# Performance work log

Measured on AMD Instinct MI355X. Metric: run time of the kernel, lower is better.

Reference implementation:

```python
import jax, jax.numpy as jnp
import numpy as np

B, L, D, NH = 4, 1500, 512, 8
HD = D // NH
EPS = 1e-8            # F.normalize eps
PEPS = 1.1920929e-07  # torch clamp_probs eps for float32
TEMP = 1.0


def setup_inputs():
    key = jax.random.key(0)
    ks = jax.random.split(key, 12)
    s = 1.0 / np.sqrt(D)
    eye = jnp.eye(D, dtype=jnp.float32)
    return {
        "hidden": jax.random.normal(ks[0], (B, L, D), jnp.float32),
        "lengths": jnp.ones((B,), jnp.float32),
        "u_noise": jax.random.uniform(ks[1], (B, L), jnp.float32),
        "W1": jax.random.normal(ks[2], (D, D), jnp.float32) * s,
        "b1": jnp.zeros((D,), jnp.float32),
        "W2": jax.random.normal(ks[3], (D, D), jnp.float32) * s,
        "b2": jnp.zeros((D,), jnp.float32),
        "Wq": eye + jax.random.normal(ks[4], (D, D), jnp.float32) * 0.01,
        "Wk": eye + jax.random.normal(ks[5], (D, D), jnp.float32) * 0.01,
        "sim_bias": jnp.float32(0.098),
        "learned_query": jax.random.normal(ks[6], (D,), jnp.float32),
        "Wpk": eye + jax.random.normal(ks[7], (D, D), jnp.float32) * 0.01,
        "Wpv": eye + jax.random.normal(ks[8], (D, D), jnp.float32) * 0.01,
        "Wpo": eye + jax.random.normal(ks[9], (D, D), jnp.float32) * 0.01,
        "ln_g": jnp.ones((D,), jnp.float32),
        "ln_b": jnp.zeros((D,), jnp.float32),
    }


def reference(hidden, lengths, u_noise, W1, b1, W2, b2, Wq, Wk, sim_bias,
              learned_query, Wpk, Wpv, Wpo, ln_g, ln_b):
    Bb, Ll, Dd = hidden.shape

    def nrm(x):
        n = jnp.sqrt(jnp.sum(x * x, -1, keepdims=True))
        return x / jnp.maximum(n, EPS)

    def mlp(x):
        return jax.nn.gelu(x @ W1.T + b1, approximate=False) @ W2.T + b2

    # boundary logits from adjacent-frame cosine similarity (dropout = eval identity)
    q_in = nrm(hidden[:, :-1]); q = nrm(mlp(q_in) + q_in) @ Wq.T
    k_in = nrm(hidden[:, 1:]);  k = nrm(mlp(k_in) + k_in) @ Wk.T
    cos = jnp.sum(q * k, -1)                                   # (B, L-1)
    probs = jnp.clip((1.0 - (cos + sim_bias)) * 0.5, 0.0, 1.0)
    probs = jnp.pad(probs, ((0, 0), (0, 1)))                   # (B, L)

    # RelaxedBernoulli rsample with explicit logistic noise
    p = jnp.clip(probs, PEPS, 1.0 - PEPS)
    u = jnp.clip(u_noise, PEPS, 1.0 - PEPS)
    soft = jax.nn.sigmoid((jnp.log(p) - jnp.log1p(-p) + jnp.log(u) - jnp.log1p(-u)) / TEMP)
    hard = (soft > 0.5).astype(hidden.dtype)

    idx = jnp.arange(Ll)
    valid_len = jnp.minimum((lengths * (Ll + 1)).astype(jnp.int32) - 1, Ll)
    trunc = (valid_len < Ll)[:, None]
    zmask = trunc & (idx[None] >= valid_len[:, None])
    omask = trunc & (idx[None] == valid_len[:, None])
    soft = jnp.where(omask, 1.0, jnp.where(zmask, 0.0, soft))
    hard = jnp.where(omask, 1.0, jnp.where(zmask, 0.0, hard))
    hard_b = hard - jax.lax.stop_gradient(soft) + soft         # straight-through
    # emergency boundary for all-zero rows
    no_b = (jnp.sum(hard, 1) == 0)[:, None]
    hard_b = jnp.where(no_b & (idx[None] == jnp.minimum(valid_len, Ll - 1)[:, None]), 1.0, hard_b)

    # segment membership (common()): token l in segment s iff exclusive cumsum == s
    seg = jnp.cumsum(hard_b, 1) - hard_b                       # (B, L)
    lmask = idx[None] < (lengths * Ll).astype(jnp.int32)[:, None]
    seg_mask = (seg[:, :, None] == idx[None, None, :].astype(hidden.dtype)) & lmask[:, :, None]  # (B,L,S)

    # layernorm + K/V projections
    mu = jnp.mean(hidden, -1, keepdims=True)
    hv = hidden - mu
    hn = hv / jnp.sqrt(jnp.mean(hv * hv, -1, keepdims=True) + 1e-5) * ln_g + ln_b
    keys = (hn @ Wpk.T).reshape(Bb, Ll, NH, HD)
    vals = (hn @ Wpv.T).reshape(Bb, Ll, NH, HD)

    # query is shared across segments -> scores only differ via the segment mask
    qh = learned_query.reshape(NH, HD)
    base = jnp.einsum('hd,blhd->bhl', qh, keys) * (HD ** -0.5)  # (B,H,L)
    mask_t = jnp.transpose(seg_mask, (0, 2, 1))[:, None]        # (B,1,S,L)
    sc = jnp.where(mask_t, base[:, :, None, :], -jnp.inf)       # (B,H,S,L)
    aw = jnp.nan_to_num(jax.nn.softmax(sc, axis=-1))            # empty segments -> 0 rows
    pooled = jnp.einsum('bhsl,blhd->bshd', aw, vals).reshape(Bb, Ll, Dd)
    return pooled @ Wpo.T                                       # (B, S=L, D)
```

## Files before the change

kernel.cpp:

```cpp
#include <hip/hip_runtime.h>
#include <math.h>

#define Bz 4
#define Lz 1500
#define Dz 512
#define NHz 8
#define Nz (Bz*Lz)
#define NRT 375
#define PEPSf 1.1920929e-07f

typedef __bf16 bf16x8 __attribute__((ext_vector_type(8)));
typedef unsigned short u16x8 __attribute__((ext_vector_type(8)));
typedef float f32x4 __attribute__((ext_vector_type(4)));
typedef unsigned short us;

__device__ __forceinline__ us f2bf(float f) {
  unsigned u = __float_as_uint(f);
  return (us)((u + 0x7fffu + ((u >> 16) & 1u)) >> 16);
}
__device__ __forceinline__ float bf2f(us b) {
  return __uint_as_float(((unsigned)b) << 16);
}
__device__ __forceinline__ void st_tiled(us* __restrict__ P, int row, int col, us v) {
  P[(((row >> 4) * 64 + (col >> 3)) << 7) + ((row & 15) << 3) + (col & 7)] = v;
}

__device__ __forceinline__ bool decode_blk(int bx, int ncg, int& R, int& cg) {
  int xcd = bx & 7, v = bx >> 3;
  cg = v % ncg;
  R = (v / ncg) * 8 + xcd;
  return R < 94;
}

__global__ __launch_bounds__(256) void k_wconv(
    const float* __restrict__ s0, const float* __restrict__ s1, const float* __restrict__ s2,
    const float* __restrict__ s3, const float* __restrict__ s4, const float* __restrict__ s5,
    us* __restrict__ h0, us* __restrict__ h1, us* __restrict__ h2,
    us* __restrict__ h3, us* __restrict__ h4, us* __restrict__ h5,
    us* __restrict__ l0, us* __restrict__ l1, us* __restrict__ l2, us* __restrict__ l3) {
  const int rt = blockIdx.x, mat = blockIdx.y, t = threadIdx.x;
  const float* S; us* H; us* L = nullptr;
  switch (mat) {
    case 0: S = s0; H = h0; L = l0; break;
    case 1: S = s1; H = h1; L = l1; break;
    case 2: S = s2; H = h2; L = l2; break;
    case 3: S = s3; H = h3; L = l3; break;
    case 4: S = s4; H = h4; break;
    default: S = s5; H = h5; break;
  }
  for (int e = t; e < 8192; e += 256) {
    int mm = e >> 9, c = e & 511;
    float x = S[(size_t)(rt * 16 + mm) * 512 + c];
    us hb = f2bf(x);
    int off = ((rt * 64 + (c >> 3)) << 7) + (mm << 3) + (c & 7);
    H[off] = hb;
    if (L) L[off] = f2bf(x - bf2f(hb));
  }
}

__global__ __launch_bounds__(256) void k_rowprep(const float* __restrict__ h,
    const float* __restrict__ g, const float* __restrict__ bb,
    float* __restrict__ U, float* __restrict__ HN,
    us* __restrict__ Uh, us* __restrict__ Ul, us* __restrict__ HNh) {
  const int row = blockIdx.x;
  const int t = threadIdx.x;
  const float* x = h + (size_t)row * Dz;
  float x0 = x[t], x1 = x[t + 256];
  float s = x0 + x1, q = x0 * x0 + x1 * x1;
  #pragma unroll
  for (int o = 32; o > 0; o >>= 1) { s += __shfl_xor(s, o, 64); q += __shfl_xor(q, o, 64); }
  __shared__ float ls[4], lq[4];
  if ((t & 63) == 0) { ls[t >> 6] = s; lq[t >> 6] = q; }
  __syncthreads();
  s = ls[0] + ls[1] + ls[2] + ls[3];
  q = lq[0] + lq[1] + lq[2] + lq[3];
  float un = 1.f / fmaxf(sqrtf(q), 1e-8f);
  float u0 = x0 * un, u1 = x1 * un;
  float* up = U + (size_t)row * Dz;
  up[t] = u0; up[t + 256] = u1;
  us hb0 = f2bf(u0), hb1 = f2bf(u1);
  st_tiled(Uh, row, t, hb0);       st_tiled(Ul, row, t, f2bf(u0 - bf2f(hb0)));
  st_tiled(Uh, row, t + 256, hb1); st_tiled(Ul, row, t + 256, f2bf(u1 - bf2f(hb1)));
  float mu = s * (1.f / 512.f);
  float var = fmaxf(q * (1.f / 512.f) - mu * mu, 0.f);
  float r = rsqrtf(var + 1e-5f);
  float hn0 = (x0 - mu) * r * g[t] + bb[t];
  float hn1 = (x1 - mu) * r * g[t + 256] + bb[t + 256];
  float* hp = HN + (size_t)row * Dz;
  hp[t] = hn0; hp[t + 256] = hn1;
  st_tiled(HNh, row, t, f2bf(hn0));
  st_tiled(HNh, row, t + 256, f2bf(hn1));
}

__global__ __launch_bounds__(256) void k_rownorm(const float* __restrict__ M,
    us* __restrict__ Vh, us* __restrict__ Vl) {
  const int row = blockIdx.x;
  const int t = threadIdx.x;
  const float* x = M + (size_t)row * Dz;
  float x0 = x[t], x1 = x[t + 256];
  float q = x0 * x0 + x1 * x1;
  #pragma unroll
  for (int o = 32; o > 0; o >>= 1) q += __shfl_xor(q, o, 64);
  __shared__ float lq[4];
  if ((t & 63) == 0) lq[t >> 6] = q;
  __syncthreads();
  q = lq[0] + lq[1] + lq[2] + lq[3];
  float un = 1.f / fmaxf(sqrtf(q), 1e-8f);
  float v0 = x0 * un, v1 = x1 * un;
  us hb0 = f2bf(v0), hb1 = f2bf(v1);
  st_tiled(Vh, row, t, hb0);       st_tiled(Vl, row, t, f2bf(v0 - bf2f(hb0)));
  st_tiled(Vh, row, t + 256, hb1); st_tiled(Vl, row, t + 256, f2bf(v1 - bf2f(hb1)));
}

template<int SPLIT>
__device__ __forceinline__ void gemm_body(
    const us* __restrict__ Ah, const us* __restrict__ Al,
    const us* __restrict__ Bh, const us* __restrict__ Bl,
    const float* __restrict__ bias, const float* __restrict__ addsrc, int doGelu,
    float* __restrict__ outF, us* __restrict__ outH, us* __restrict__ outL,
    int R, int cg, int colbase) {
  const int t = threadIdx.x, w = t >> 6, l = t & 63;
  const int m = l & 15, q = l >> 4;
  const int rt0 = R * 4;
  const int ct0 = cg * 8 + w * 2;
  const int laneoff = q * 128 + m * 8;

  const u16x8* pa[4]; const u16x8* pal[4];
  const u16x8* pb[2]; const u16x8* pbl[2];
  #pragma unroll
  for (int i = 0; i < 4; ++i) {
    int rt = min(rt0 + i, NRT - 1);
    pa[i] = (const u16x8*)(Ah + (size_t)rt * 8192 + laneoff);
    if (SPLIT == 3) pal[i] = (const u16x8*)(Al + (size_t)rt * 8192 + laneoff);
  }
  #pragma unroll
  for (int j = 0; j < 2; ++j) {
    pb[j] = (const u16x8*)(Bh + (size_t)(ct0 + j) * 8192 + laneoff);
    if (SPLIT == 3) pbl[j] = (const u16x8*)(Bl + (size_t)(ct0 + j) * 8192 + laneoff);
  }

  u16x8 bAh[2][4], bAl[2][4], bBh[2][2], bBl[2][2];
  #pragma unroll
  for (int i = 0; i < 4; ++i) {
    bAh[0][i] = pa[i][0];
    if (SPLIT == 3) bAl[0][i] = pal[i][0];
  }
  #pragma unroll
  for (int j = 0; j < 2; ++j) {
    bBh[0][j] = pb[j][0];
    if (SPLIT == 3) bBl[0][j] = pbl[j][0];
  }

  f32x4 acc[4][2];
  #pragma unroll
  for (int i = 0; i < 4; ++i)
    #pragma unroll
    for (int j = 0; j < 2; ++j) acc[i][j] = (f32x4){0.f, 0.f, 0.f, 0.f};

  #pragma unroll 2
  for (int s = 0; s < 16; ++s) {
    const int cur = s & 1, nxt = cur ^ 1;
    const int sn = (s + 1) & 15;
    #pragma unroll
    for (int i = 0; i < 4; ++i) {
      bAh[nxt][i] = pa[i][sn * 64];
      if (SPLIT == 3) bAl[nxt][i] = pal[i][sn * 64];
    }
    #pragma unroll
    for (int j = 0; j < 2; ++j) {
      bBh[nxt][j] = pb[j][sn * 64];
      if (SPLIT == 3) bBl[nxt][j] = pbl[j][sn * 64];
    }
    #pragma unroll
    for (int i = 0; i < 4; ++i)
      #pragma unroll
      for (int j = 0; j < 2; ++j) {
        bf16x8 a = __builtin_bit_cast(bf16x8, bAh[cur][i]);
        bf16x8 b = __builtin_bit_cast(bf16x8, bBh[cur][j]);
        acc[i][j] = __builtin_amdgcn_mfma_f32_16x16x32_bf16(a, b, acc[i][j], 0, 0, 0);
        if (SPLIT == 3) {
          bf16x8 al_ = __builtin_bit_cast(bf16x8, bAl[cur][i]);
          bf16x8 bl_ = __builtin_bit_cast(bf16x8, bBl[cur][j]);
          acc[i][j] = __builtin_amdgcn_mfma_f32_16x16x32_bf16(a, bl_, acc[i][j], 0, 0, 0);
          acc[i][j] = __builtin_amdgcn_mfma_f32_16x16x32_bf16(al_, b, acc[i][j], 0, 0, 0);
        }
      }
  }

  const int row0 = rt0 * 16;
  #pragma unroll
  for (int i = 0; i < 4; ++i) {
    #pragma unroll
    for (int r = 0; r < 4; ++r) {
      const int grow = row0 + i * 16 + q * 4 + r;
      if (grow >= Nz) continue;
      #pragma unroll
      for (int j = 0; j < 2; ++j) {
        const int gcol = colbase + (w * 2 + j) * 16 + m;
        float v = acc[i][j][r];
        if (bias)   v += bias[gcol];
        if (addsrc) v += addsrc[(size_t)grow * Dz + gcol];
        if (doGelu) v = 0.5f * v * (1.f + erff(v * 0.70710678118654752f));
        if (outF) outF[(size_t)grow * Dz + gcol] = v;
        if (outH) {
          us hb = f2bf(v);
          st_tiled(outH, grow, gcol, hb);
          if (outL) st_tiled(outL, grow, gcol, f2bf(v - bf2f(hb)));
        }
      }
    }
  }
}

__global__ __launch_bounds__(256, 2) void g_t1_vals(
    const us* Uh, const us* Ul, const us* W1h, const us* W1l, const float* b1, us* T1h, us* T1l,
    const us* HNh, const us* Wpvh, float* VALS) {
  int R, cg;
  if (!decode_blk(blockIdx.x, 4, R, cg)) return;
  if (blockIdx.z == 0)
    gemm_body<3>(Uh, Ul, W1h, W1l, b1, nullptr, 1, nullptr, T1h, T1l, R, cg, cg * 128);
  else
    gemm_body<1>(HNh, nullptr, Wpvh, nullptr, nullptr, nullptr, 0, VALS, nullptr, nullptr, R, cg, cg * 128);
}

__global__ __launch_bounds__(256, 2) void g_w2(
    const us* T1h, const us* T1l, const us* W2h, const us* W2l, const float* b2,
    const float* U, float* M) {
  int R, cg;
  if (!decode_blk(blockIdx.x, 4, R, cg)) return;
  gemm_body<3>(T1h, T1l, W2h, W2l, b2, U, 0, M, nullptr, nullptr, R, cg, cg * 128);
}

__global__ __launch_bounds__(256, 2) void g_qk(
    const us* Vh, const us* Vl, const us* Wqh, const us* Wql, const us* Wkh, const us* Wkl,
    float* QF, float* KF) {
  int R, cg;
  if (!decode_blk(blockIdx.x, 8, R, cg)) return;
  if (cg < 4)
    gemm_body<3>(Vh, Vl, Wqh, Wql, nullptr, nullptr, 0, QF, nullptr, nullptr, R, cg & 3, (cg & 3) * 128);
  else
    gemm_body<3>(Vh, Vl, Wkh, Wkl, nullptr, nullptr, 0, KF, nullptr, nullptr, R, cg & 3, (cg & 3) * 128);
}

__global__ __launch_bounds__(256, 2) void g_out(
    const us* Ph, const us* Wpoh, float* out) {
  int R, cg;
  if (!decode_blk(blockIdx.x, 4, R, cg)) return;
  gemm_body<1>(Ph, nullptr, Wpoh, nullptr, nullptr, nullptr, 0, out, nullptr, nullptr, R, cg, cg * 128);
}

__global__ void k_probs(const float* __restrict__ QF, const float* __restrict__ KF,
                        const float* __restrict__ simb, float* __restrict__ probs) {
  const int l = blockIdx.x, b = blockIdx.y, t = threadIdx.x;
  if (l == Lz - 1) { if (t == 0) probs[(size_t)b * Lz + l] = 0.f; return; }
  const float* qp = QF + ((size_t)b * Lz + l) * Dz;
  const float* kp = KF + ((size_t)b * Lz + l + 1) * Dz;
  float acc = 0.f;
  for (int i = t; i < Dz; i += 64) acc += qp[i] * kp[i];
  #pragma unroll
  for (int o = 32; o > 0; o >>= 1) acc += __shfl_xor(acc, o, 64);
  if (t == 0) {
    float p = (1.f - (acc + simb[0])) * 0.5f;
    probs[(size_t)b * Lz + l] = fminf(fmaxf(p, 0.f), 1.f);
  }
}

__global__ __launch_bounds__(256) void k_boundary(const float* __restrict__ probs,
    const float* __restrict__ un, const float* __restrict__ lengths,
    int* __restrict__ seg_start, int* __restrict__ seg_meta) {
  const int b = blockIdx.x, t = threadIdx.x;
  __shared__ float hard[Lz];
  __shared__ float ps[256];
  __shared__ float ws4[4];
  const float len = lengths[b];
  const int valid_len = min((int)(len * (Lz + 1)) - 1, Lz);
  const int Lm = (int)(len * Lz);
  const bool trunc = valid_len < Lz;
  for (int l = t; l < Lz; l += 256) {
    float p = probs[(size_t)b * Lz + l];
    p = fminf(fmaxf(p, PEPSf), 1.f - PEPSf);
    float u = un[(size_t)b * Lz + l];
    u = fminf(fmaxf(u, PEPSf), 1.f - PEPSf);
    float z = logf(p) - log1pf(-p) + logf(u) - log1pf(-u);
    float soft = 1.f / (1.f + expf(-z));
    float hd = soft > 0.5f ? 1.f : 0.f;
    if (trunc && l >= valid_len) hd = (l == valid_len) ? 1.f : 0.f;
    hard[l] = hd;
  }
  __syncthreads();
  float sm = 0.f;
  for (int l = t; l < Lz; l += 256) sm += hard[l];
  #pragma unroll
  for (int o = 32; o > 0; o >>= 1) sm += __shfl_xor(sm, o, 64);
  if ((t & 63) == 0) ws4[t >> 6] = sm;
  __syncthreads();
  float total = ws4[0] + ws4[1] + ws4[2] + ws4[3];
  if (total == 0.f && t == 0) hard[min(valid_len, Lz - 1)] = 1.f;
  __syncthreads();
  const int l0 = t * 6;
  float loc = 0.f;
  for (int i = 0; i < 6; ++i) { int l = l0 + i; if (l < Lz) loc += hard[l]; }
  ps[t] = loc;
  __syncthreads();
  for (int off = 1; off < 256; off <<= 1) {
    float v = (t >= off) ? ps[t - off] : 0.f;
    __syncthreads();
    ps[t] += v;
    __syncthreads();
  }
  float run = ps[t] - loc;
  for (int i = 0; i < 6; ++i) {
    int l = l0 + i; if (l >= Lz) break;
    int seg = (int)(run + 0.5f);
    if (l == 0) seg_start[b * (Lz + 1) + 0] = 0;
    else if (hard[l - 1] > 0.5f) seg_start[b * (Lz + 1) + seg] = l;
    if (l == Lz - 1) {
      int nseg = seg + 1;
      seg_meta[b * 2 + 0] = nseg;
      seg_meta[b * 2 + 1] = Lm;
      seg_start[b * (Lz + 1) + nseg] = Lz;
    }
    run += hard[l];
  }
}

__global__ void k_wqeff(const float* __restrict__ lq, const float* __restrict__ Wpk,
                        float* __restrict__ wqe) {
  const int h = blockIdx.x, d = threadIdx.x;
  float acc = 0.f;
  for (int e = 0; e < 64; ++e) acc += lq[h * 64 + e] * Wpk[(size_t)(h * 64 + e) * Dz + d];
  wqe[h * Dz + d] = acc;
}

__global__ __launch_bounds__(256) void k_base(const float* __restrict__ HN,
    const float* __restrict__ wqe, float* __restrict__ base) {
  const int row = blockIdx.x, t = threadIdx.x;
  __shared__ float xs[Dz];
  xs[t] = HN[(size_t)row * Dz + t];
  xs[t + 256] = HN[(size_t)row * Dz + t + 256];
  __syncthreads();
  const int h = t >> 5, lane = t & 31;
  float acc = 0.f;
  for (int d = lane; d < Dz; d += 32) acc += xs[d] * wqe[h * Dz + d];
  #pragma unroll
  for (int o = 16; o > 0; o >>= 1) acc += __shfl_xor(acc, o, 32);
  if (lane == 0) base[(size_t)row * NHz + h] = acc * 0.125f;
}

__global__ __launch_bounds__(256) void k_pool(const float* __restrict__ base,
    const float* __restrict__ VALS, const int* __restrict__ seg_start,
    const int* __restrict__ seg_meta, us* __restrict__ Ph) {
  const int s = blockIdx.x, b = blockIdx.y, t = threadIdx.x;
  const int orow = b * Lz + s;
  const int nseg = seg_meta[b * 2], Lm = seg_meta[b * 2 + 1];
  int start = 0, end = 0;
  bool empty = true;
  if (s < nseg) {
    start = seg_start[b * (Lz + 1) + s];
    end = min(seg_start[b * (Lz + 1) + s + 1], Lm);
    empty = start >= end;
  }
  if (empty) { st_tiled(Ph, orow, t, 0); st_tiled(Ph, orow, t + 256, 0); return; }
  const int h = t >> 5, lane = t & 31;
  const float* bp = base + (size_t)b * Lz * NHz + h;
  float m = -1e30f;
  for (int l = start + lane; l < end; l += 32) m = fmaxf(m, bp[(size_t)l * NHz]);
  #pragma unroll
  for (int o = 16; o > 0; o >>= 1) m = fmaxf(m, __shfl_xor(m, o, 32));
  float den = 0.f;
  for (int l = start + lane; l < end; l += 32) den += expf(bp[(size_t)l * NHz] - m);
  #pragma unroll
  for (int o = 16; o > 0; o >>= 1) den += __shfl_xor(den, o, 32);
  float a0 = 0.f, a1 = 0.f;
  const float* vp = VALS + (size_t)b * Lz * Dz + h * 64 + lane;
  for (int l = start; l < end; ++l) {
    float wgt = expf(bp[(size_t)l * NHz] - m);
    a0 += wgt * vp[(size_t)l * Dz];
    a1 += wgt * vp[(size_t)l * Dz + 32];
  }
  float inv = 1.f / den;
  st_tiled(Ph, orow, h * 64 + lane, f2bf(a0 * inv));
  st_tiled(Ph, orow, h * 64 + lane + 32, f2bf(a1 * inv));
}

extern "C" void kernel_launch(void* const* d_in, const int* in_sizes, int n_in,
                              void* d_out, int out_size, void* d_ws, size_t ws_size,
                              hipStream_t stream) {
  const float* hidden  = (const float*)d_in[0];
  const float* lengths = (const float*)d_in[1];
  const float* unoise  = (const float*)d_in[2];
  const float* W1  = (const float*)d_in[3];
  const float* b1  = (const float*)d_in[4];
  const float* W2  = (const float*)d_in[5];
  const float* b2  = (const float*)d_in[6];
  const float* Wq  = (const float*)d_in[7];
  const float* Wk  = (const float*)d_in[8];
  const float* simb   = (const float*)d_in[9];
  const float* lquery = (const float*)d_in[10];
  const float* Wpk = (const float*)d_in[11];
  const float* Wpv = (const float*)d_in[12];
  const float* Wpo = (const float*)d_in[13];
  const float* lng = (const float*)d_in[14];
  const float* lnb = (const float*)d_in[15];
  float* out = (float*)d_out;

  char* p = (char*)d_ws;
  const size_t SF = (size_t)Nz * Dz * 4;
  const size_t TP = (size_t)376 * 8192 * 2;
  const size_t WP = (size_t)32 * 8192 * 2;
  float* U    = (float*)p; p += SF;
  float* HN   = (float*)p; p += SF;
  float* M    = (float*)p; p += SF;
  float* QF   = (float*)p; p += SF;
  float* KF   = (float*)p; p += SF;
  float* VALS = (float*)p; p += SF;
  us* Uh  = (us*)p; p += TP;
  us* Ul  = (us*)p; p += TP;
  us* T1h = (us*)p; p += TP;
  us* T1l = (us*)p; p += TP;
  us* Vh  = (us*)p; p += TP;
  us* Vl  = (us*)p; p += TP;
  us* HNh = (us*)p; p += TP;
  us* Ph  = (us*)p; p += TP;
  us* W1h = (us*)p; p += WP;
  us* W1l = (us*)p; p += WP;
  us* W2h = (us*)p; p += WP;
  us* W2l = (us*)p; p += WP;
  us* Wqh = (us*)p; p += WP;
  us* Wql = (us*)p; p += WP;
  us* Wkh = (us*)p; p += WP;
  us* Wkl = (us*)p; p += WP;
  us* Wpvh = (us*)p; p += WP;
  us* Wpoh = (us*)p; p += WP;
  float* probs  = (float*)p; p += 24064;
  float* base   = (float*)p; p += 192000;
  int* segst    = (int*)p;   p += 24064;
  int* segmeta  = (int*)p;   p += 256;
  float* wqe    = (float*)p;

  const int G4 = 8 * 12 * 4;
  const int G8 = 8 * 12 * 8;

  k_wconv<<<dim3(32, 6), 256, 0, stream>>>(W1, W2, Wq, Wk, Wpv, Wpo,
      W1h, W2h, Wqh, Wkh, Wpvh, Wpoh, W1l, W2l, Wql, Wkl);
  k_wqeff<<<NHz, 512, 0, stream>>>(lquery, Wpk, wqe);
  k_rowprep<<<Nz, 256, 0, stream>>>(hidden, lng, lnb, U, HN, Uh, Ul, HNh);
  g_t1_vals<<<dim3(G4, 1, 2), 256, 0, stream>>>(Uh, Ul, W1h, W1l, b1, T1h, T1l,
                                                HNh, Wpvh, VALS);
  g_w2<<<G4, 256, 0, stream>>>(T1h, T1l, W2h, W2l, b2, U, M);
  k_rownorm<<<Nz, 256, 0, stream>>>(M, Vh, Vl);
  g_qk<<<G8, 256, 0, stream>>>(Vh, Vl, Wqh, Wql, Wkh, Wkl, QF, KF);
  k_probs<<<dim3(Lz, Bz), 64, 0, stream>>>(QF, KF, simb, probs);
  k_boundary<<<Bz, 256, 0, stream>>>(probs, unoise, lengths, segst, segmeta);
  k_base<<<Nz, 256, 0, stream>>>(HN, wqe, base);
  k_pool<<<dim3(Lz, Bz), 256, 0, stream>>>(base, VALS, segst, segmeta, Ph);
  g_out<<<G4, 256, 0, stream>>>(Ph, Wpoh, out);
}
```

Measured before the change: 262.0 us.

## Fold Wq and Wk into one Gram matrix and fuse base into rowprep

Rewrites cos = (Wq v_l)·(Wk v_{l+1}) as v_l·(Wq^T Wk) M_{l+1}·rn. A small 512x512 GEMM precomputes G = Wq^T Wk, so the two large Q/K projection GEMMs become one GEMM plus a scaled dot with the unnormalized M. The k_base head-score reduction moves into k_rowprep, and the wqe computation moves into the weight conversion kernel, which removes two launches and a reread of HN. Launch bounds rise to 3 blocks per CU, and the extra bf16-split rounding of G may shift the probabilities near the hard threshold.

```diff
diff --git a/kernel.cpp b/kernel.cpp
--- a/kernel.cpp
+++ b/kernel.cpp
@@ -6,7 +6,6 @@
 #define Dz 512
 #define NHz 8
 #define Nz (Bz*Lz)
-#define NRT 375
 #define PEPSf 1.1920929e-07f
 
 typedef __bf16 bf16x8 __attribute__((ext_vector_type(8)));
@@ -34,23 +33,37 @@
 
 __global__ __launch_bounds__(256) void k_wconv(
     const float* __restrict__ s0, const float* __restrict__ s1, const float* __restrict__ s2,
-    const float* __restrict__ s3, const float* __restrict__ s4, const float* __restrict__ s5,
-    us* __restrict__ h0, us* __restrict__ h1, us* __restrict__ h2,
-    us* __restrict__ h3, us* __restrict__ h4, us* __restrict__ h5,
-    us* __restrict__ l0, us* __restrict__ l1, us* __restrict__ l2, us* __restrict__ l3) {
+    const float* __restrict__ s3,
+    const float* __restrict__ Wq, const float* __restrict__ Wk,
+    const float* __restrict__ Wpk, const float* __restrict__ lq,
+    us* __restrict__ h0, us* __restrict__ h1, us* __restrict__ h2, us* __restrict__ h3,
+    us* __restrict__ l0, us* __restrict__ l1,
+    us* __restrict__ WkTh, us* __restrict__ WkTl, us* __restrict__ WqTh, us* __restrict__ WqTl,
+    float* __restrict__ wqe) {
   const int rt = blockIdx.x, mat = blockIdx.y, t = threadIdx.x;
-  const float* S; us* H; us* L = nullptr;
+  if (mat == 8) {
+    if (rt < 8) {
+      for (int d = t; d < Dz; d += 256) {
+        float acc = 0.f;
+        for (int e = 0; e < 64; ++e) acc += lq[rt * 64 + e] * Wpk[(size_t)(rt * 64 + e) * Dz + d];
+        wqe[rt * Dz + d] = acc;
+      }
+    }
+    return;
+  }
+  const float* S; us* H; us* L = nullptr; bool tr = false;
   switch (mat) {
     case 0: S = s0; H = h0; L = l0; break;
     case 1: S = s1; H = h1; L = l1; break;
-    case 2: S = s2; H = h2; L = l2; break;
-    case 3: S = s3; H = h3; L = l3; break;
-    case 4: S = s4; H = h4; break;
-    default: S = s5; H = h5; break;
+    case 2: S = s2; H = h2; break;
+    case 3: S = s3; H = h3; break;
+    case 4: S = Wk; H = WkTh; L = WkTl; tr = true; break;
+    default: S = Wq; H = WqTh; L = WqTl; tr = true; break;
   }
   for (int e = t; e < 8192; e += 256) {
     int mm = e >> 9, c = e & 511;
-    float x = S[(size_t)(rt * 16 + mm) * 512 + c];
+    float x = tr ? S[(size_t)c * 512 + (rt * 16 + mm)]
+                 : S[(size_t)(rt * 16 + mm) * 512 + c];
     us hb = f2bf(x);
     int off = ((rt * 64 + (c >> 3)) << 7) + (mm << 3) + (c & 7);
     H[off] = hb;
@@ -60,8 +73,10 @@
 
 __global__ __launch_bounds__(256) void k_rowprep(const float* __restrict__ h,
     const float* __restrict__ g, const float* __restrict__ bb,
+    const float* __restrict__ wqe,
     float* __restrict__ U, float* __restrict__ HN,
-    us* __restrict__ Uh, us* __restrict__ Ul, us* __restrict__ HNh) {
+    us* __restrict__ Uh, us* __restrict__ Ul, us* __restrict__ HNh,
+    float* __restrict__ base) {
   const int row = blockIdx.x;
   const int t = threadIdx.x;
   const float* x = h + (size_t)row * Dz;
@@ -70,6 +85,7 @@
   #pragma unroll
   for (int o = 32; o > 0; o >>= 1) { s += __shfl_xor(s, o, 64); q += __shfl_xor(q, o, 64); }
   __shared__ float ls[4], lq[4];
+  __shared__ float xs[Dz];
   if ((t & 63) == 0) { ls[t >> 6] = s; lq[t >> 6] = q; }
   __syncthreads();
   s = ls[0] + ls[1] + ls[2] + ls[3];
@@ -90,10 +106,18 @@
   hp[t] = hn0; hp[t + 256] = hn1;
   st_tiled(HNh, row, t, f2bf(hn0));
   st_tiled(HNh, row, t + 256, f2bf(hn1));
+  xs[t] = hn0; xs[t + 256] = hn1;
+  __syncthreads();
+  const int hh = t >> 5, lane = t & 31;
+  float accb = 0.f;
+  for (int d = lane; d < Dz; d += 32) accb += xs[d] * wqe[hh * Dz + d];
+  #pragma unroll
+  for (int o = 16; o > 0; o >>= 1) accb += __shfl_xor(accb, o, 32);
+  if (lane == 0) base[(size_t)row * NHz + hh] = accb * 0.125f;
 }
 
 __global__ __launch_bounds__(256) void k_rownorm(const float* __restrict__ M,
-    us* __restrict__ Vh, us* __restrict__ Vl) {
+    us* __restrict__ Vh, us* __restrict__ Vl, float* __restrict__ rn) {
   const int row = blockIdx.x;
   const int t = threadIdx.x;
   const float* x = M + (size_t)row * Dz;
@@ -106,6 +130,7 @@
   __syncthreads();
   q = lq[0] + lq[1] + lq[2] + lq[3];
   float un = 1.f / fmaxf(sqrtf(q), 1e-8f);
+  if (t == 0) rn[row] = un;
   float v0 = x0 * un, v1 = x1 * un;
   us hb0 = f2bf(v0), hb1 = f2bf(v1);
   st_tiled(Vh, row, t, hb0);       st_tiled(Vl, row, t, f2bf(v0 - bf2f(hb0)));
@@ -118,18 +143,19 @@
     const us* __restrict__ Bh, const us* __restrict__ Bl,
     const float* __restrict__ bias, const float* __restrict__ addsrc, int doGelu,
     float* __restrict__ outF, us* __restrict__ outH, us* __restrict__ outL,
-    int R, int cg, int colbase) {
+    int R, int cg, int colbase, int Nrows) {
   const int t = threadIdx.x, w = t >> 6, l = t & 63;
   const int m = l & 15, q = l >> 4;
   const int rt0 = R * 4;
   const int ct0 = cg * 8 + w * 2;
   const int laneoff = q * 128 + m * 8;
+  const int nrtm1 = (Nrows >> 4) - 1;
 
   const u16x8* pa[4]; const u16x8* pal[4];
   const u16x8* pb[2]; const u16x8* pbl[2];
   #pragma unroll
   for (int i = 0; i < 4; ++i) {
-    int rt = min(rt0 + i, NRT - 1);
+    int rt = min(rt0 + i, nrtm1);
     pa[i] = (const u16x8*)(Ah + (size_t)rt * 8192 + laneoff);
     if (SPLIT == 3) pal[i] = (const u16x8*)(Al + (size_t)rt * 8192 + laneoff);
   }
@@ -193,7 +219,7 @@
     #pragma unroll
     for (int r = 0; r < 4; ++r) {
       const int grow = row0 + i * 16 + q * 4 + r;
-      if (grow >= Nz) continue;
+      if (grow >= Nrows) continue;
       #pragma unroll
       for (int j = 0; j < 2; ++j) {
         const int gcol = colbase + (w * 2 + j) * 16 + m;
@@ -212,55 +238,60 @@
   }
 }
 
-__global__ __launch_bounds__(256, 2) void g_t1_vals(
+__global__ __launch_bounds__(256, 2) void g_gt(
+    const us* WkTh, const us* WkTl, const us* WqTh, const us* WqTl,
+    us* Gth, us* Gtl) {
+  gemm_body<3>(WkTh, WkTl, WqTh, WqTl, nullptr, nullptr, 0, nullptr, Gth, Gtl,
+               blockIdx.y, blockIdx.x, blockIdx.x * 128, 512);
+}
+
+__global__ __launch_bounds__(256, 3) void g_t1_vals(
     const us* Uh, const us* Ul, const us* W1h, const us* W1l, const float* b1, us* T1h, us* T1l,
     const us* HNh, const us* Wpvh, float* VALS) {
   int R, cg;
   if (!decode_blk(blockIdx.x, 4, R, cg)) return;
   if (blockIdx.z == 0)
-    gemm_body<3>(Uh, Ul, W1h, W1l, b1, nullptr, 1, nullptr, T1h, T1l, R, cg, cg * 128);
+    gemm_body<3>(Uh, Ul, W1h, W1l, b1, nullptr, 1, nullptr, T1h, T1l, R, cg, cg * 128, Nz);
   else
-    gemm_body<1>(HNh, nullptr, Wpvh, nullptr, nullptr, nullptr, 0, VALS, nullptr, nullptr, R, cg, cg * 128);
-}
-
-__global__ __launch_bounds__(256, 2) void g_w2(
+    gemm_body<1>(HNh, nullptr, Wpvh, nullptr, nullptr, nullptr, 0, VALS, nullptr, nullptr, R, cg, cg * 128, Nz);
+}
+
+__global__ __launch_bounds__(256, 3) void g_w2(
     const us* T1h, const us* T1l, const us* W2h, const us* W2l, const float* b2,
     const float* U, float* M) {
   int R, cg;
   if (!decode_blk(blockIdx.x, 4, R, cg)) return;
-  gemm_body<3>(T1h, T1l, W2h, W2l, b2, U, 0, M, nullptr, nullptr, R, cg, cg * 128);
-}
-
-__global__ __launch_bounds__(256, 2) void g_qk(
-    const us* Vh, const us* Vl, const us* Wqh, const us* Wql, const us* Wkh, const us* Wkl,
-    float* QF, float* KF) {
+  gemm_body<3>(T1h, T1l, W2h, W2l, b2, U, 0, M, nullptr, nullptr, R, cg, cg * 128, Nz);
+}
+
+__global__ __launch_bounds__(256, 3) void g_p(
+    const us* Vh, const us* Vl, const us* Gth, const us* Gtl, float* P) {
   int R, cg;
-  if (!decode_blk(blockIdx.x, 8, R, cg)) return;
-  if (cg < 4)
-    gemm_body<3>(Vh, Vl, Wqh, Wql, nullptr, nullptr, 0, QF, nullptr, nullptr, R, cg & 3, (cg & 3) * 128);
-  else
-    gemm_body<3>(Vh, Vl, Wkh, Wkl, nullptr, nullptr, 0, KF, nullptr, nullptr, R, cg & 3, (cg & 3) * 128);
-}
-
-__global__ __launch_bounds__(256, 2) void g_out(
+  if (!decode_blk(blockIdx.x, 4, R, cg)) return;
+  gemm_body<3>(Vh, Vl, Gth, Gtl, nullptr, nullptr, 0, P, nullptr, nullptr, R, cg, cg * 128, Nz);
+}
+
+__global__ __launch_bounds__(256, 3) void g_out(
     const us* Ph, const us* Wpoh, float* out) {
   int R, cg;
   if (!decode_blk(blockIdx.x, 4, R, cg)) return;
-  gemm_body<1>(Ph, nullptr, Wpoh, nullptr, nullptr, nullptr, 0, out, nullptr, nullptr, R, cg, cg * 128);
-}
-
-__global__ void k_probs(const float* __restrict__ QF, const float* __restrict__ KF,
+  gemm_body<1>(Ph, nullptr, Wpoh, nullptr, nullptr, nullptr, 0, out, nullptr, nullptr, R, cg, cg * 128, Nz);
+}
+
+__global__ void k_probs(const float* __restrict__ P, const float* __restrict__ M,
+                        const float* __restrict__ rn,
                         const float* __restrict__ simb, float* __restrict__ probs) {
   const int l = blockIdx.x, b = blockIdx.y, t = threadIdx.x;
   if (l == Lz - 1) { if (t == 0) probs[(size_t)b * Lz + l] = 0.f; return; }
-  const float* qp = QF + ((size_t)b * Lz + l) * Dz;
-  const float* kp = KF + ((size_t)b * Lz + l + 1) * Dz;
+  const float* pp = P + ((size_t)b * Lz + l) * Dz;
+  const float* mp = M + ((size_t)b * Lz + l + 1) * Dz;
   float acc = 0.f;
-  for (int i = t; i < Dz; i += 64) acc += qp[i] * kp[i];
+  for (int i = t; i < Dz; i += 64) acc += pp[i] * mp[i];
   #pragma unroll
   for (int o = 32; o > 0; o >>= 1) acc += __shfl_xor(acc, o, 64);
   if (t == 0) {
-    float p = (1.f - (acc + simb[0])) * 0.5f;
+    float cosv = acc * rn[(size_t)b * Lz + l + 1];
+    float p = (1.f - (cosv + simb[0])) * 0.5f;
     probs[(size_t)b * Lz + l] = fminf(fmaxf(p, 0.f), 1.f);
   }
 }
@@ -324,29 +355,6 @@
   }
 }
 
-__global__ void k_wqeff(const float* __restrict__ lq, const float* __restrict__ Wpk,
-                        float* __restrict__ wqe) {
-  const int h = blockIdx.x, d = threadIdx.x;
-  float acc = 0.f;
-  for (int e = 0; e < 64; ++e) acc += lq[h * 64 + e] * Wpk[(size_t)(h * 64 + e) * Dz + d];
-  wqe[h * Dz + d] = acc;
-}
-
-__global__ __launch_bounds__(256) void k_base(const float* __restrict__ HN,
-    const float* __restrict__ wqe, float* __restrict__ base) {
-  const int row = blockIdx.x, t = threadIdx.x;
-  __shared__ float xs[Dz];
-  xs[t] = HN[(size_t)row * Dz + t];
-  xs[t + 256] = HN[(size_t)row * Dz + t + 256];
-  __syncthreads();
-  const int h = t >> 5, lane = t & 31;
-  float acc = 0.f;
-  for (int d = lane; d < Dz; d += 32) acc += xs[d] * wqe[h * Dz + d];
-  #pragma unroll
-  for (int o = 16; o > 0; o >>= 1) acc += __shfl_xor(acc, o, 32);
-  if (lane == 0) base[(size_t)row * NHz + h] = acc * 0.125f;
-}
-
 __global__ __launch_bounds__(256) void k_pool(const float* __restrict__ base,
     const float* __restrict__ VALS, const int* __restrict__ seg_start,
     const int* __restrict__ seg_meta, us* __restrict__ Ph) {
@@ -411,8 +419,7 @@
   float* U    = (float*)p; p += SF;
   float* HN   = (float*)p; p += SF;
   float* M    = (float*)p; p += SF;
-  float* QF   = (float*)p; p += SF;
-  float* KF   = (float*)p; p += SF;
+  float* PF   = (float*)p; p += SF;
   float* VALS = (float*)p; p += SF;
   us* Uh  = (us*)p; p += TP;
   us* Ul  = (us*)p; p += TP;
@@ -426,33 +433,34 @@
   us* W1l = (us*)p; p += WP;
   us* W2h = (us*)p; p += WP;
   us* W2l = (us*)p; p += WP;
-  us* Wqh = (us*)p; p += WP;
-  us* Wql = (us*)p; p += WP;
-  us* Wkh = (us*)p; p += WP;
-  us* Wkl = (us*)p; p += WP;
   us* Wpvh = (us*)p; p += WP;
   us* Wpoh = (us*)p; p += WP;
+  us* WkTh = (us*)p; p += WP;
+  us* WkTl = (us*)p; p += WP;
+  us* WqTh = (us*)p; p += WP;
+  us* WqTl = (us*)p; p += WP;
+  us* Gth  = (us*)p; p += WP;
+  us* Gtl  = (us*)p; p += WP;
   float* probs  = (float*)p; p += 24064;
   float* base   = (float*)p; p += 192000;
+  float* rn     = (float*)p; p += 24064;
   int* segst    = (int*)p;   p += 24064;
   int* segmeta  = (int*)p;   p += 256;
   float* wqe    = (float*)p;
 
   const int G4 = 8 * 12 * 4;
-  const int G8 = 8 * 12 * 8;
-
-  k_wconv<<<dim3(32, 6), 256, 0, stream>>>(W1, W2, Wq, Wk, Wpv, Wpo,
-      W1h, W2h, Wqh, Wkh, Wpvh, Wpoh, W1l, W2l, Wql, Wkl);
-  k_wqeff<<<NHz, 512, 0, stream>>>(lquery, Wpk, wqe);
-  k_rowprep<<<Nz, 256, 0, stream>>>(hidden, lng, lnb, U, HN, Uh, Ul, HNh);
+
+  k_wconv<<<dim3(32, 9), 256, 0, stream>>>(W1, W2, Wpv, Wpo, Wq, Wk, Wpk, lquery,
+      W1h, W2h, Wpvh, Wpoh, W1l, W2l, WkTh, WkTl, WqTh, WqTl, wqe);
+  k_rowprep<<<Nz, 256, 0, stream>>>(hidden, lng, lnb, wqe, U, HN, Uh, Ul, HNh, base);
+  g_gt<<<dim3(4, 8), 256, 0, stream>>>(WkTh, WkTl, WqTh, WqTl, Gth, Gtl);
   g_t1_vals<<<dim3(G4, 1, 2), 256, 0, stream>>>(Uh, Ul, W1h, W1l, b1, T1h, T1l,
                                                 HNh, Wpvh, VALS);
   g_w2<<<G4, 256, 0, stream>>>(T1h, T1l, W2h, W2l, b2, U, M);
-  k_rownorm<<<Nz, 256, 0, stream>>>(M, Vh, Vl);
-  g_qk<<<G8, 256, 0, stream>>>(Vh, Vl, Wqh, Wql, Wkh, Wkl, QF, KF);
-  k_probs<<<dim3(Lz, Bz), 64, 0, stream>>>(QF, KF, simb, probs);
+  k_rownorm<<<Nz, 256, 0, stream>>>(M, Vh, Vl, rn);
+  g_p<<<G4, 256, 0, stream>>>(Vh, Vl, Gth, Gtl, PF);
+  k_probs<<<dim3(Lz, Bz), 64, 0, stream>>>(PF, M, rn, simb, probs);
   k_boundary<<<Bz, 256, 0, stream>>>(probs, unoise, lengths, segst, segmeta);
-  k_base<<<Nz, 256, 0, stream>>>(HN, wqe, base);
   k_pool<<<dim3(Lz, Bz), 256, 0, stream>>>(base, VALS, segst, segmeta, Ph);
   g_out<<<G4, 256, 0, stream>>>(Ph, Wpoh, out);
 }
```

Result: slower. 270.2 us (+3.1%).
